# Optimization experiments

Hardware: AMD Instinct MI355X
Metric: run time of the kernel (lower is better)

The kernel has to match this reference:

```python
import jax, jax.numpy as jnp
import numpy as np

N = 512
D = 512
# static upper-triangle pair indices (i < j)
_II, _JJ = np.triu_indices(N, k=1)
_II = jnp.asarray(_II)
_JJ = jnp.asarray(_JJ)


def setup_inputs() -> dict:
    key = jax.random.key(0)
    ks = jax.random.split(key, 9)
    s = 0.02
    return {
        'features': jax.random.normal(ks[0], (N, D), dtype=jnp.float32),
        # relation_classifier: Linear(2D->D), Linear(D->10)
        'cw1': jax.random.normal(ks[1], (2 * D, D), dtype=jnp.float32) * s,
        'cb1': jnp.zeros((D,), dtype=jnp.float32),
        'cw2': jax.random.normal(ks[2], (D, 10), dtype=jnp.float32) * s,
        'cb2': jnp.zeros((10,), dtype=jnp.float32),
        # relation_strength_calc: Linear(2D->D//2), Linear(D//2->1)
        'sw1': jax.random.normal(ks[3], (2 * D, D // 2), dtype=jnp.float32) * s,
        'sb1': jnp.zeros((D // 2,), dtype=jnp.float32),
        'sw2': jax.random.normal(ks[4], (D // 2, 1), dtype=jnp.float32) * s,
        'sb2': jnp.zeros((1,), dtype=jnp.float32),
    }


def reference(features, cw1, cb1, cw2, cb2, sw1, sb1, sw2, sb2):
    # cat([f_i, f_j]) @ W == f_i @ W[:D] + f_j @ W[D:]  (linear-split trick)
    # precompute per-node projections once, then gather per pair
    c_a = features @ cw1[:D]   # [N, D]
    c_b = features @ cw1[D:]   # [N, D]
    s_a = features @ sw1[:D]   # [N, D//2]
    s_b = features @ sw1[D:]   # [N, D//2]

    # classifier path
    h = jax.nn.relu(c_a[_II] + c_b[_JJ] + cb1)          # [P, D]
    relation_types = jax.nn.log_softmax(h @ cw2 + cb2)   # [P, 10]
    most_likely_relations = jnp.argmax(relation_types, axis=-1)  # [P]

    # strength path
    hs = jax.nn.relu(s_a[_II] + s_b[_JJ] + sb1)          # [P, D//2]
    relation_strengths = jax.nn.sigmoid(hs @ sw2 + sb2)   # [P, 1]

    return relation_types, most_likely_relations, relation_strengths
```

## Files before the change

kernel.cpp:

```cpp
#include <hip/hip_runtime.h>
#include <math.h>

#define NN 512
#define DD 512
#define NPAIRS 130816
#define TYPES_OFF 0
#define ARGMAX_OFF 1308160
#define STRENGTH_OFF 1438976


__global__ __launch_bounds__(256) void init_ws_kernel(
    const float* __restrict__ cb1, const float* __restrict__ sb1,
    const float* __restrict__ cw2,
    double* __restrict__ ca_d, double* __restrict__ cb_d,
    float* __restrict__ sa_f, float* __restrict__ sb_f,
    double* __restrict__ cw2d)
{
    int idx = blockIdx.x * 256 + threadIdx.x;
    ca_d[idx] = (double)cb1[idx & 511];
    cb_d[idx] = 0.0;
    if (idx < 131072) {
        sa_f[idx] = sb1[idx & 255];
        sb_f[idx] = 0.f;
    }
    if (idx < 5120) cw2d[idx] = (double)cw2[idx];
}

__global__ __launch_bounds__(256, 4) void proj_kernel(
    const float* __restrict__ F, const float* __restrict__ cw1,
    const float* __restrict__ sw1,
    double* __restrict__ ca_d, double* __restrict__ cb_d,
    float* __restrict__ sa_f, float* __restrict__ sb_f)
{
    __shared__ double sh[2 * 16 * 66];

    const int t = threadIdx.x;
    const int b = blockIdx.x;

    const int am = t & 63, aq = t >> 6;
    const int br = t >> 4, bq = t & 15;
    const int ty = t >> 4, tx = t & 15;

    if (b < 256) {
        const int z  = b >> 7;
        const int r  = b & 127;
        const int m0 = (r >> 4) * 64;
        const int ng = (r & 15) * 64;
        const float* Bp  = (ng < 512) ? cw1 : cw1 + 512 * 512;
        double* outp     = (ng < 512) ? ca_d : cb_d;
        const int coloff = (ng < 512) ? ng : ng - 512;

        double* As = sh;
        double* Bs = sh + 16 * 66;

        double acc[4][4];
        #pragma unroll
        for (int r2 = 0; r2 < 4; ++r2)
            #pragma unroll
            for (int c2 = 0; c2 < 4; ++c2) acc[r2][c2] = 0.0;

        for (int k0 = z * 256; k0 < z * 256 + 256; k0 += 16) {
            float4 fa = *(const float4*)&F [(m0 + am) * 512 + k0 + aq * 4];
            float4 fb = *(const float4*)&Bp[(k0 + br) * 512 + coloff + bq * 4];
            __syncthreads();
            As[(aq * 4 + 0) * 66 + am] = (double)fa.x;
            As[(aq * 4 + 1) * 66 + am] = (double)fa.y;
            As[(aq * 4 + 2) * 66 + am] = (double)fa.z;
            As[(aq * 4 + 3) * 66 + am] = (double)fa.w;
            double2* bd = (double2*)&Bs[br * 66 + bq * 4];
            bd[0] = make_double2((double)fb.x, (double)fb.y);
            bd[1] = make_double2((double)fb.z, (double)fb.w);
            __syncthreads();
            #pragma unroll
            for (int kk = 0; kk < 16; ++kk) {
                double2 a0 = *(double2*)&As[kk * 66 + ty * 4];
                double2 a1 = *(double2*)&As[kk * 66 + ty * 4 + 2];
                double2 b0 = *(double2*)&Bs[kk * 66 + tx * 4];
                double2 b1 = *(double2*)&Bs[kk * 66 + tx * 4 + 2];
                double av[4] = {a0.x, a0.y, a1.x, a1.y};
                double bv[4] = {b0.x, b0.y, b1.x, b1.y};
                #pragma unroll
                for (int r2 = 0; r2 < 4; ++r2)
                    #pragma unroll
                    for (int c2 = 0; c2 < 4; ++c2)
                        acc[r2][c2] = fma(av[r2], bv[c2], acc[r2][c2]);
            }
        }
        #pragma unroll
        for (int r2 = 0; r2 < 4; ++r2)
            #pragma unroll
            for (int c2 = 0; c2 < 4; ++c2)
                unsafeAtomicAdd(&outp[(m0 + ty * 4 + r2) * 512 + coloff + tx * 4 + c2],
                                acc[r2][c2]);
    } else {
        const int b2 = b - 256;
        const int z  = b2 >> 6;
        const int r  = b2 & 63;
        const int m0 = (r >> 3) * 64;
        const int ng = (r & 7) * 64;
        const float* Bp  = (ng < 256) ? sw1 : sw1 + 512 * 256;
        float* outp      = (ng < 256) ? sa_f : sb_f;
        const int coloff = (ng < 256) ? ng : ng - 256;

        float* Asf = (float*)sh;
        float* Bsf = (float*)sh + 16 * 68;

        float acc[4][4];
        #pragma unroll
        for (int r2 = 0; r2 < 4; ++r2)
            #pragma unroll
            for (int c2 = 0; c2 < 4; ++c2) acc[r2][c2] = 0.f;

        for (int k0 = z * 256; k0 < z * 256 + 256; k0 += 16) {
            float4 fa = *(const float4*)&F [(m0 + am) * 512 + k0 + aq * 4];
            float4 fb = *(const float4*)&Bp[(k0 + br) * 256 + coloff + bq * 4];
            __syncthreads();
            Asf[(aq * 4 + 0) * 68 + am] = fa.x;
            Asf[(aq * 4 + 1) * 68 + am] = fa.y;
            Asf[(aq * 4 + 2) * 68 + am] = fa.z;
            Asf[(aq * 4 + 3) * 68 + am] = fa.w;
            *(float4*)&Bsf[br * 68 + bq * 4] = fb;
            __syncthreads();
            #pragma unroll
            for (int kk = 0; kk < 16; ++kk) {
                float4 a4 = *(float4*)&Asf[kk * 68 + ty * 4];
                float4 b4 = *(float4*)&Bsf[kk * 68 + tx * 4];
                float av[4] = {a4.x, a4.y, a4.z, a4.w};
                float bv[4] = {b4.x, b4.y, b4.z, b4.w};
                #pragma unroll
                for (int r2 = 0; r2 < 4; ++r2)
                    #pragma unroll
                    for (int c2 = 0; c2 < 4; ++c2)
                        acc[r2][c2] = fmaf(av[r2], bv[c2], acc[r2][c2]);
            }
        }
        #pragma unroll
        for (int r2 = 0; r2 < 4; ++r2)
            #pragma unroll
            for (int c2 = 0; c2 < 4; ++c2)
                unsafeAtomicAdd(&outp[(m0 + ty * 4 + r2) * 256 + coloff + tx * 4 + c2],
                                acc[r2][c2]);
    }
}

__global__ __launch_bounds__(256, 4) void pair_kernel(
    const double* __restrict__ ca_d, const double* __restrict__ cb_d,
    const float* __restrict__ sa_f, const float* __restrict__ sb_f,
    const double* __restrict__ cw2d, const float* __restrict__ cb2,
    const float* __restrict__ sw2, const float* __restrict__ sb2,
    float* __restrict__ out)
{
    const int b = blockIdx.x;
    int bi = (int)floorf((129.0f - sqrtf(16641.0f - 8.0f * (float)b)) * 0.5f);
    while ((bi + 1) * (129 - (bi + 1)) / 2 <= b) ++bi;
    while (bi * (129 - bi) / 2 > b) --bi;
    const int bj = bi + (b - bi * (129 - bi) / 2);
    const int i0 = bi * 8, j0 = bj * 8;

    const int t = threadIdx.x;
    const int q  = t >> 6;
    const int qu = __builtin_amdgcn_readfirstlane(q);
    const int l = t & 63;
    const int pi = l >> 3, pj = l & 7;
    const int i = i0 + pi, j = j0 + pj;

    __shared__ double smem_d[2176];
    double* sA  = smem_d;
    double* sB  = smem_d + 1088;
    float*  sSa = (float*)smem_d;
    float*  sSb = (float*)smem_d + 2176;
    double* lgbuf = smem_d;
    float*  stbuf = (float*)(smem_d + 1920);

    #pragma unroll
    for (int u = 0; u < 4; ++u) {
        int idx = u * 256 + t;
        int kq  = idx & 15;
        int row = (idx >> 4) & 7;
        int qq  = (idx >> 7) & 3;
        int arr = idx >> 9;
        const float* src = arr ? (sb_f + (j0 + row) * 256) : (sa_f + (i0 + row) * 256);
        float4 v = *(const float4*)(src + qq * 64 + kq * 4);
        float* dst = (arr ? sSb : sSa) + (qq * 8 + row) * 68 + kq * 4;
        *(float4*)dst = v;
    }
    __syncthreads();
    float accs = 0.f;
    {
        const float* sw2q = sw2 + qu * 64;
        const float* ra = sSa + (q * 8 + pi) * 68;
        const float* rb = sSb + (q * 8 + pj) * 68;
        #pragma unroll 16
        for (int kk = 0; kk < 64; ++kk) {
            float h = fmaxf(ra[kk] + rb[kk], 0.f);
            accs = fmaf(h, sw2q[kk], accs);
        }
    }

    double lg[10];
    #pragma unroll
    for (int c = 0; c < 10; ++c) lg[c] = 0.0;
    const double* wq = cw2d + qu * 1280;

    for (int c4 = 0; c4 < 4; ++c4) {
        __syncthreads();
        #pragma unroll
        for (int u = 0; u < 4; ++u) {
            int idx = u * 256 + t;
            int kq  = idx & 15;
            int row = (idx >> 4) & 7;
            int qq  = (idx >> 7) & 3;
            int arr = idx >> 9;
            const double* src = arr ? (cb_d + (j0 + row) * 512) : (ca_d + (i0 + row) * 512);
            double2 v = *(const double2*)(src + qq * 128 + c4 * 32 + kq * 2);
            double* dst = (arr ? sB : sA) + (qq * 8 + row) * 34 + kq * 2;
            *(double2*)dst = v;
        }
        __syncthreads();
        const double* ra = sA + (q * 8 + pi) * 34;
        const double* rb = sB + (q * 8 + pj) * 34;
        const double* wc = wq + c4 * 320;
        #pragma unroll 8
        for (int kk = 0; kk < 32; ++kk) {
            double h = fmax(ra[kk] + rb[kk], 0.0);
            const double* w = wc + kk * 10;
            #pragma unroll
            for (int c = 0; c < 10; ++c) lg[c] = fma(h, w[c], lg[c]);
        }
    }

    __syncthreads();
    if (q > 0) {
        double* dst = lgbuf + ((q - 1) * 64 + l) * 10;
        #pragma unroll
        for (int c = 0; c < 10; ++c) dst[c] = lg[c];
        stbuf[(q - 1) * 64 + l] = accs;
    }
    __syncthreads();
    if (q == 0) {
        #pragma unroll
        for (int w = 0; w < 3; ++w) {
            const double* srcb = lgbuf + (w * 64 + l) * 10;
            #pragma unroll
            for (int c = 0; c < 10; ++c) lg[c] += srcb[c];
        }
        float st = accs + stbuf[l] + stbuf[64 + l] + stbuf[128 + l] + sb2[0];

        #pragma unroll
        for (int c = 0; c < 10; ++c) lg[c] += (double)cb2[c];
        double mx = lg[0]; int am2 = 0;
        #pragma unroll
        for (int c = 1; c < 10; ++c) {
            if (lg[c] > mx) { mx = lg[c]; am2 = c; }
        }
        float tf[10]; float s = 0.f;
        #pragma unroll
        for (int c = 0; c < 10; ++c) { tf[c] = (float)(lg[c] - mx); s += __expf(tf[c]); }
        float ls = __logf(s);

        if (j > i) {
            const int p = i * 511 - (i * (i - 1)) / 2 + (j - i - 1);
            float* tp = out + TYPES_OFF + p * 10;
            #pragma unroll
            for (int c = 0; c < 10; ++c) tp[c] = tf[c] - ls;
            out[ARGMAX_OFF + p] = (float)am2;
            out[STRENGTH_OFF + p] = 1.0f / (1.0f + __expf(-st));
        }
    }
}

extern "C" void kernel_launch(void* const* d_in, const int* in_sizes, int n_in,
                              void* d_out, int out_size, void* d_ws, size_t ws_size,
                              hipStream_t stream) {
    const float* F   = (const float*)d_in[0];
    const float* cw1 = (const float*)d_in[1];
    const float* cb1 = (const float*)d_in[2];
    const float* cw2 = (const float*)d_in[3];
    const float* cb2 = (const float*)d_in[4];
    const float* sw1 = (const float*)d_in[5];
    const float* sb1 = (const float*)d_in[6];
    const float* sw2 = (const float*)d_in[7];
    const float* sb2 = (const float*)d_in[8];
    float* out = (float*)d_out;

    char* ws = (char*)d_ws;
    double* ca_d = (double*)(ws);
    double* cb_d = (double*)(ws + 2097152);
    float*  sa_f = (float*)(ws + 4194304);
    float*  sb_f = (float*)(ws + 4718592);
    double* cw2d = (double*)(ws + 5242880);

    hipLaunchKernelGGL(init_ws_kernel, dim3(1024), dim3(256), 0, stream,
                       cb1, sb1, cw2, ca_d, cb_d, sa_f, sb_f, cw2d);
    hipLaunchKernelGGL(proj_kernel, dim3(384), dim3(256), 0, stream,
                       F, cw1, sw1, ca_d, cb_d, sa_f, sb_f);
    hipLaunchKernelGGL(pair_kernel, dim3(2080), dim3(256), 0, stream,
                       ca_d, cb_d, sa_f, sb_f, cw2d, cb2, sw2, sb2, out);
}
```

Baseline: 164.0 us.

## Drop init kernel and atomics; split-K partials summed in pair kernel

Removes the workspace init kernel and the atomic accumulation in the projection GEMM. Each split-K half now writes its own partial buffer with plain stores, the bias is added in the z=0 half, and the pair kernel sums the two partials when it loads tiles. The projection is rewritten as a per-wave register-tiled GEMM that reads operands straight from global memory with software prefetch instead of going through LDS. This saves one launch and the atomic traffic, but doubles the projection bytes the pair kernel reads and drops LDS reuse in the GEMM.

```diff
diff --git a/kernel.cpp b/kernel.cpp
--- a/kernel.cpp
+++ b/kernel.cpp
@@ -9,143 +9,182 @@
 #define STRENGTH_OFF 1438976
 
 
-__global__ __launch_bounds__(256) void init_ws_kernel(
-    const float* __restrict__ cb1, const float* __restrict__ sb1,
-    const float* __restrict__ cw2,
-    double* __restrict__ ca_d, double* __restrict__ cb_d,
-    float* __restrict__ sa_f, float* __restrict__ sb_f,
-    double* __restrict__ cw2d)
+__device__ __forceinline__ void fma64_step(
+    const float4& a0, const float4& a1,
+    const float4& b0, const float4& b1, const float4& b2, const float4& b3,
+    double acc[2][4])
 {
-    int idx = blockIdx.x * 256 + threadIdx.x;
-    ca_d[idx] = (double)cb1[idx & 511];
-    cb_d[idx] = 0.0;
-    if (idx < 131072) {
-        sa_f[idx] = sb1[idx & 255];
-        sb_f[idx] = 0.f;
-    }
-    if (idx < 5120) cw2d[idx] = (double)cw2[idx];
+    const float av[2][4] = {{a0.x,a0.y,a0.z,a0.w},{a1.x,a1.y,a1.z,a1.w}};
+    const float bv[4][4] = {{b0.x,b0.y,b0.z,b0.w},{b1.x,b1.y,b1.z,b1.w},
+                            {b2.x,b2.y,b2.z,b2.w},{b3.x,b3.y,b3.z,b3.w}};
+    #pragma unroll
+    for (int kk = 0; kk < 4; ++kk) {
+        double ad0 = (double)av[0][kk], ad1 = (double)av[1][kk];
+        #pragma unroll
+        for (int c = 0; c < 4; ++c) {
+            double bd = (double)bv[kk][c];
+            acc[0][c] = fma(ad0, bd, acc[0][c]);
+            acc[1][c] = fma(ad1, bd, acc[1][c]);
+        }
+    }
+}
+
+__device__ __forceinline__ void fma32_step(
+    const float4& a0, const float4& a1,
+    const float4& b0, const float4& b1, const float4& b2, const float4& b3,
+    float acc[2][4])
+{
+    const float av[2][4] = {{a0.x,a0.y,a0.z,a0.w},{a1.x,a1.y,a1.z,a1.w}};
+    const float bv[4][4] = {{b0.x,b0.y,b0.z,b0.w},{b1.x,b1.y,b1.z,b1.w},
+                            {b2.x,b2.y,b2.z,b2.w},{b3.x,b3.y,b3.z,b3.w}};
+    #pragma unroll
+    for (int kk = 0; kk < 4; ++kk) {
+        #pragma unroll
+        for (int c = 0; c < 4; ++c) {
+            acc[0][c] = fmaf(av[0][kk], bv[kk][c], acc[0][c]);
+            acc[1][c] = fmaf(av[1][kk], bv[kk][c], acc[1][c]);
+        }
+    }
 }
 
 __global__ __launch_bounds__(256, 4) void proj_kernel(
     const float* __restrict__ F, const float* __restrict__ cw1,
     const float* __restrict__ sw1,
-    double* __restrict__ ca_d, double* __restrict__ cb_d,
-    float* __restrict__ sa_f, float* __restrict__ sb_f)
+    const float* __restrict__ cb1, const float* __restrict__ sb1,
+    const float* __restrict__ cw2,
+    double* __restrict__ ca0, double* __restrict__ ca1,
+    double* __restrict__ cb0, double* __restrict__ cbp1,
+    float* __restrict__ sa0, float* __restrict__ sa1,
+    float* __restrict__ sb0, float* __restrict__ sbp1,
+    double* __restrict__ cw2d)
 {
-    __shared__ double sh[2 * 16 * 66];
-
     const int t = threadIdx.x;
-    const int b = blockIdx.x;
-
-    const int am = t & 63, aq = t >> 6;
-    const int br = t >> 4, bq = t & 15;
-    const int ty = t >> 4, tx = t & 15;
-
-    if (b < 256) {
-        const int z  = b >> 7;
-        const int r  = b & 127;
-        const int m0 = (r >> 4) * 64;
-        const int ng = (r & 15) * 64;
-        const float* Bp  = (ng < 512) ? cw1 : cw1 + 512 * 512;
-        double* outp     = (ng < 512) ? ca_d : cb_d;
-        const int coloff = (ng < 512) ? ng : ng - 512;
-
-        double* As = sh;
-        double* Bs = sh + 16 * 66;
-
-        double acc[4][4];
-        #pragma unroll
-        for (int r2 = 0; r2 < 4; ++r2)
-            #pragma unroll
-            for (int c2 = 0; c2 < 4; ++c2) acc[r2][c2] = 0.0;
-
-        for (int k0 = z * 256; k0 < z * 256 + 256; k0 += 16) {
-            float4 fa = *(const float4*)&F [(m0 + am) * 512 + k0 + aq * 4];
-            float4 fb = *(const float4*)&Bp[(k0 + br) * 512 + coloff + bq * 4];
-            __syncthreads();
-            As[(aq * 4 + 0) * 66 + am] = (double)fa.x;
-            As[(aq * 4 + 1) * 66 + am] = (double)fa.y;
-            As[(aq * 4 + 2) * 66 + am] = (double)fa.z;
-            As[(aq * 4 + 3) * 66 + am] = (double)fa.w;
-            double2* bd = (double2*)&Bs[br * 66 + bq * 4];
-            bd[0] = make_double2((double)fb.x, (double)fb.y);
-            bd[1] = make_double2((double)fb.z, (double)fb.w);
-            __syncthreads();
-            #pragma unroll
-            for (int kk = 0; kk < 16; ++kk) {
-                double2 a0 = *(double2*)&As[kk * 66 + ty * 4];
-                double2 a1 = *(double2*)&As[kk * 66 + ty * 4 + 2];
-                double2 b0 = *(double2*)&Bs[kk * 66 + tx * 4];
-                double2 b1 = *(double2*)&Bs[kk * 66 + tx * 4 + 2];
-                double av[4] = {a0.x, a0.y, a1.x, a1.y};
-                double bv[4] = {b0.x, b0.y, b1.x, b1.y};
-                #pragma unroll
-                for (int r2 = 0; r2 < 4; ++r2)
-                    #pragma unroll
-                    for (int c2 = 0; c2 < 4; ++c2)
-                        acc[r2][c2] = fma(av[r2], bv[c2], acc[r2][c2]);
+    if (blockIdx.x >= 768) {
+        int idx = (blockIdx.x - 768) * 256 + t;
+        if (idx < 5120) cw2d[idx] = (double)cw2[idx];
+        return;
+    }
+    const int wid  = blockIdx.x * 4 + (t >> 6);
+    const int lane = t & 63;
+    const int mg = lane >> 4;
+    const int nq = lane & 15;
+
+    if (wid < 2048) {
+        const int z  = wid & 1;
+        const int r  = wid >> 1;
+        const int nt = r & 15;
+        const int mt = r >> 4;
+        const int m0 = mt * 8;
+        const int n  = nt * 64;
+        const float* W = (n < 512) ? cw1 : cw1 + 512 * 512;
+        const int n0   = (n < 512) ? n : n - 512;
+        double* outp   = (n < 512) ? (z ? ca1 : ca0) : (z ? cbp1 : cb0);
+        const bool addbias = (z == 0) && (n < 512);
+
+        const int row0 = m0 + mg * 2;
+        const int col0 = n0 + nq * 4;
+        const float* pa0 = F + row0 * 512 + z * 256;
+        const float* pa1 = pa0 + 512;
+        const float* pb  = W + (z * 256) * 512 + col0;
+
+        double acc[2][4];
+        #pragma unroll
+        for (int rr = 0; rr < 2; ++rr)
+            #pragma unroll
+            for (int cc = 0; cc < 4; ++cc) acc[rr][cc] = 0.0;
+
+        float4 a0 = *(const float4*)(pa0);
+        float4 a1 = *(const float4*)(pa1);
+        float4 b0 = *(const float4*)(pb);
+        float4 b1 = *(const float4*)(pb + 512);
+        float4 b2 = *(const float4*)(pb + 1024);
+        float4 b3 = *(const float4*)(pb + 1536);
+        for (int s = 0; s < 63; ++s) {
+            float4 na0 = *(const float4*)(pa0 + (s + 1) * 4);
+            float4 na1 = *(const float4*)(pa1 + (s + 1) * 4);
+            const float* nb = pb + (s + 1) * 2048;
+            float4 nb0 = *(const float4*)(nb);
+            float4 nb1 = *(const float4*)(nb + 512);
+            float4 nb2 = *(const float4*)(nb + 1024);
+            float4 nb3 = *(const float4*)(nb + 1536);
+            fma64_step(a0, a1, b0, b1, b2, b3, acc);
+            a0 = na0; a1 = na1; b0 = nb0; b1 = nb1; b2 = nb2; b3 = nb3;
+        }
+        fma64_step(a0, a1, b0, b1, b2, b3, acc);
+
+        #pragma unroll
+        for (int rr = 0; rr < 2; ++rr) {
+            double v[4];
+            #pragma unroll
+            for (int cc = 0; cc < 4; ++cc) {
+                v[cc] = acc[rr][cc];
+                if (addbias) v[cc] += (double)cb1[col0 + cc];
             }
-        }
-        #pragma unroll
-        for (int r2 = 0; r2 < 4; ++r2)
-            #pragma unroll
-            for (int c2 = 0; c2 < 4; ++c2)
-                unsafeAtomicAdd(&outp[(m0 + ty * 4 + r2) * 512 + coloff + tx * 4 + c2],
-                                acc[r2][c2]);
+            double* dst = outp + (row0 + rr) * 512 + col0;
+            *(double2*)(dst + 0) = make_double2(v[0], v[1]);
+            *(double2*)(dst + 2) = make_double2(v[2], v[3]);
+        }
     } else {
-        const int b2 = b - 256;
-        const int z  = b2 >> 6;
-        const int r  = b2 & 63;
-        const int m0 = (r >> 3) * 64;
-        const int ng = (r & 7) * 64;
-        const float* Bp  = (ng < 256) ? sw1 : sw1 + 512 * 256;
-        float* outp      = (ng < 256) ? sa_f : sb_f;
-        const int coloff = (ng < 256) ? ng : ng - 256;
-
-        float* Asf = (float*)sh;
-        float* Bsf = (float*)sh + 16 * 68;
-
-        float acc[4][4];
-        #pragma unroll
-        for (int r2 = 0; r2 < 4; ++r2)
-            #pragma unroll
-            for (int c2 = 0; c2 < 4; ++c2) acc[r2][c2] = 0.f;
-
-        for (int k0 = z * 256; k0 < z * 256 + 256; k0 += 16) {
-            float4 fa = *(const float4*)&F [(m0 + am) * 512 + k0 + aq * 4];
-            float4 fb = *(const float4*)&Bp[(k0 + br) * 256 + coloff + bq * 4];
-            __syncthreads();
-            Asf[(aq * 4 + 0) * 68 + am] = fa.x;
-            Asf[(aq * 4 + 1) * 68 + am] = fa.y;
-            Asf[(aq * 4 + 2) * 68 + am] = fa.z;
-            Asf[(aq * 4 + 3) * 68 + am] = fa.w;
-            *(float4*)&Bsf[br * 68 + bq * 4] = fb;
-            __syncthreads();
-            #pragma unroll
-            for (int kk = 0; kk < 16; ++kk) {
-                float4 a4 = *(float4*)&Asf[kk * 68 + ty * 4];
-                float4 b4 = *(float4*)&Bsf[kk * 68 + tx * 4];
-                float av[4] = {a4.x, a4.y, a4.z, a4.w};
-                float bv[4] = {b4.x, b4.y, b4.z, b4.w};
-                #pragma unroll
-                for (int r2 = 0; r2 < 4; ++r2)
-                    #pragma unroll
-                    for (int c2 = 0; c2 < 4; ++c2)
-                        acc[r2][c2] = fmaf(av[r2], bv[c2], acc[r2][c2]);
+        const int w2 = wid - 2048;
+        const int z  = w2 & 1;
+        const int r  = w2 >> 1;
+        const int nt = r & 7;
+        const int mt = r >> 3;
+        const int m0 = mt * 8;
+        const int n  = nt * 64;
+        const float* W = (n < 256) ? sw1 : sw1 + 512 * 256;
+        const int n0   = (n < 256) ? n : n - 256;
+        float* outp    = (n < 256) ? (z ? sa1 : sa0) : (z ? sbp1 : sb0);
+        const bool addbias = (z == 0) && (n < 256);
+
+        const int row0 = m0 + mg * 2;
+        const int col0 = n0 + nq * 4;
+        const float* pa0 = F + row0 * 512 + z * 256;
+        const float* pa1 = pa0 + 512;
+        const float* pb  = W + (z * 256) * 256 + col0;
+
+        float acc[2][4];
+        #pragma unroll
+        for (int rr = 0; rr < 2; ++rr)
+            #pragma unroll
+            for (int cc = 0; cc < 4; ++cc) acc[rr][cc] = 0.f;
+
+        float4 a0 = *(const float4*)(pa0);
+        float4 a1 = *(const float4*)(pa1);
+        float4 b0 = *(const float4*)(pb);
+        float4 b1 = *(const float4*)(pb + 256);
+        float4 b2 = *(const float4*)(pb + 512);
+        float4 b3 = *(const float4*)(pb + 768);
+        for (int s = 0; s < 63; ++s) {
+            float4 na0 = *(const float4*)(pa0 + (s + 1) * 4);
+            float4 na1 = *(const float4*)(pa1 + (s + 1) * 4);
+            const float* nb = pb + (s + 1) * 1024;
+            float4 nb0 = *(const float4*)(nb);
+            float4 nb1 = *(const float4*)(nb + 256);
+            float4 nb2 = *(const float4*)(nb + 512);
+            float4 nb3 = *(const float4*)(nb + 768);
+            fma32_step(a0, a1, b0, b1, b2, b3, acc);
+            a0 = na0; a1 = na1; b0 = nb0; b1 = nb1; b2 = nb2; b3 = nb3;
+        }
+        fma32_step(a0, a1, b0, b1, b2, b3, acc);
+
+        #pragma unroll
+        for (int rr = 0; rr < 2; ++rr) {
+            float4 v = make_float4(acc[rr][0], acc[rr][1], acc[rr][2], acc[rr][3]);
+            if (addbias) {
+                v.x += sb1[col0 + 0]; v.y += sb1[col0 + 1];
+                v.z += sb1[col0 + 2]; v.w += sb1[col0 + 3];
             }
-        }
-        #pragma unroll
-        for (int r2 = 0; r2 < 4; ++r2)
-            #pragma unroll
-            for (int c2 = 0; c2 < 4; ++c2)
-                unsafeAtomicAdd(&outp[(m0 + ty * 4 + r2) * 256 + coloff + tx * 4 + c2],
-                                acc[r2][c2]);
+            *(float4*)(outp + (row0 + rr) * 256 + col0) = v;
+        }
     }
 }
 
 __global__ __launch_bounds__(256, 4) void pair_kernel(
-    const double* __restrict__ ca_d, const double* __restrict__ cb_d,
-    const float* __restrict__ sa_f, const float* __restrict__ sb_f,
+    const double* __restrict__ ca0, const double* __restrict__ ca1,
+    const double* __restrict__ cb0, const double* __restrict__ cbp1,
+    const float* __restrict__ sa0, const float* __restrict__ sa1,
+    const float* __restrict__ sb0, const float* __restrict__ sbp1,
     const double* __restrict__ cw2d, const float* __restrict__ cb2,
     const float* __restrict__ sw2, const float* __restrict__ sb2,
     float* __restrict__ out)
@@ -179,8 +218,12 @@
         int row = (idx >> 4) & 7;
         int qq  = (idx >> 7) & 3;
         int arr = idx >> 9;
-        const float* src = arr ? (sb_f + (j0 + row) * 256) : (sa_f + (i0 + row) * 256);
-        float4 v = *(const float4*)(src + qq * 64 + kq * 4);
+        int off = (arr ? (j0 + row) : (i0 + row)) * 256 + qq * 64 + kq * 4;
+        const float* s0 = arr ? sb0 : sa0;
+        const float* s1 = arr ? sbp1 : sa1;
+        float4 v0 = *(const float4*)(s0 + off);
+        float4 v1 = *(const float4*)(s1 + off);
+        float4 v = make_float4(v0.x + v1.x, v0.y + v1.y, v0.z + v1.z, v0.w + v1.w);
         float* dst = (arr ? sSb : sSa) + (qq * 8 + row) * 68 + kq * 4;
         *(float4*)dst = v;
     }
@@ -211,8 +254,12 @@
             int row = (idx >> 4) & 7;
             int qq  = (idx >> 7) & 3;
             int arr = idx >> 9;
-            const double* src = arr ? (cb_d + (j0 + row) * 512) : (ca_d + (i0 + row) * 512);
-            double2 v = *(const double2*)(src + qq * 128 + c4 * 32 + kq * 2);
+            int off = (arr ? (j0 + row) : (i0 + row)) * 512 + qq * 128 + c4 * 32 + kq * 2;
+            const double* d0 = arr ? cb0 : ca0;
+            const double* d1 = arr ? cbp1 : ca1;
+            double2 u0 = *(const double2*)(d0 + off);
+            double2 u1 = *(const double2*)(d1 + off);
+            double2 v = make_double2(u0.x + u1.x, u0.y + u1.y);
             double* dst = (arr ? sB : sA) + (qq * 8 + row) * 34 + kq * 2;
             *(double2*)dst = v;
         }
@@ -284,16 +331,20 @@
     float* out = (float*)d_out;
 
     char* ws = (char*)d_ws;
-    double* ca_d = (double*)(ws);
-    double* cb_d = (double*)(ws + 2097152);
-    float*  sa_f = (float*)(ws + 4194304);
-    float*  sb_f = (float*)(ws + 4718592);
-    double* cw2d = (double*)(ws + 5242880);
-
-    hipLaunchKernelGGL(init_ws_kernel, dim3(1024), dim3(256), 0, stream,
-                       cb1, sb1, cw2, ca_d, cb_d, sa_f, sb_f, cw2d);
-    hipLaunchKernelGGL(proj_kernel, dim3(384), dim3(256), 0, stream,
-                       F, cw1, sw1, ca_d, cb_d, sa_f, sb_f);
+    double* ca0  = (double*)(ws);
+    double* ca1  = (double*)(ws + 2097152);
+    double* cb0  = (double*)(ws + 4194304);
+    double* cbp1 = (double*)(ws + 6291456);
+    float*  sa0  = (float*)(ws + 8388608);
+    float*  sa1  = (float*)(ws + 8912896);
+    float*  sb0  = (float*)(ws + 9437184);
+    float*  sbp1 = (float*)(ws + 9961472);
+    double* cw2d = (double*)(ws + 10485760);
+
+    hipLaunchKernelGGL(proj_kernel, dim3(788), dim3(256), 0, stream,
+                       F, cw1, sw1, cb1, sb1, cw2,
+                       ca0, ca1, cb0, cbp1, sa0, sa1, sb0, sbp1, cw2d);
     hipLaunchKernelGGL(pair_kernel, dim3(2080), dim3(256), 0, stream,
-                       ca_d, cb_d, sa_f, sb_f, cw2d, cb2, sw2, sb2, out);
-}
+                       ca0, ca1, cb0, cbp1, sa0, sa1, sb0, sbp1,
+                       cw2d, cb2, sw2, sb2, out);
+}
```

Result: faster. 153.1 us (-6.6%).

## Fuse workspace init into projection GEMM, drop split-K atomics, prefetch pair tiles

Applied to the files above, without the earlier changes.

Removes the init kernel by folding the bias add and cw2 double conversion into the projection kernel. The projection GEMM switches from a split-K shared-memory tiled scheme with atomic accumulation to per-wave register tiles that read global memory directly, with a two-stage software-pipelined load, and writes results with plain stores. The pair kernel now prefetches the next chunk of double projections into registers while computing the current one. In exchange there is less data reuse through LDS in the GEMM, and the occupancy hint drops to two blocks.

```diff
diff --git a/kernel.cpp b/kernel.cpp
--- a/kernel.cpp
+++ b/kernel.cpp
@@ -9,137 +9,153 @@
 #define STRENGTH_OFF 1438976
 
 
-__global__ __launch_bounds__(256) void init_ws_kernel(
+struct StageC { float4 a0, a1, b0, b1, b2, b3; };
+
+__device__ __forceinline__ void fma64_step(const StageC& s, double acc[2][4]) {
+    const float av[2][4] = {{s.a0.x,s.a0.y,s.a0.z,s.a0.w},{s.a1.x,s.a1.y,s.a1.z,s.a1.w}};
+    const float bv[4][4] = {{s.b0.x,s.b0.y,s.b0.z,s.b0.w},{s.b1.x,s.b1.y,s.b1.z,s.b1.w},
+                            {s.b2.x,s.b2.y,s.b2.z,s.b2.w},{s.b3.x,s.b3.y,s.b3.z,s.b3.w}};
+    #pragma unroll
+    for (int kk = 0; kk < 4; ++kk) {
+        double ad0 = (double)av[0][kk], ad1 = (double)av[1][kk];
+        #pragma unroll
+        for (int c = 0; c < 4; ++c) {
+            double bd = (double)bv[kk][c];
+            acc[0][c] = fma(ad0, bd, acc[0][c]);
+            acc[1][c] = fma(ad1, bd, acc[1][c]);
+        }
+    }
+}
+
+__device__ __forceinline__ void fma32_step(const StageC& s, float acc[2][4]) {
+    const float av[2][4] = {{s.a0.x,s.a0.y,s.a0.z,s.a0.w},{s.a1.x,s.a1.y,s.a1.z,s.a1.w}};
+    const float bv[4][4] = {{s.b0.x,s.b0.y,s.b0.z,s.b0.w},{s.b1.x,s.b1.y,s.b1.z,s.b1.w},
+                            {s.b2.x,s.b2.y,s.b2.z,s.b2.w},{s.b3.x,s.b3.y,s.b3.z,s.b3.w}};
+    #pragma unroll
+    for (int kk = 0; kk < 4; ++kk) {
+        #pragma unroll
+        for (int c = 0; c < 4; ++c) {
+            acc[0][c] = fmaf(av[0][kk], bv[kk][c], acc[0][c]);
+            acc[1][c] = fmaf(av[1][kk], bv[kk][c], acc[1][c]);
+        }
+    }
+}
+
+__global__ __launch_bounds__(256, 2) void proj_kernel(
+    const float* __restrict__ F, const float* __restrict__ cw1,
+    const float* __restrict__ sw1,
     const float* __restrict__ cb1, const float* __restrict__ sb1,
     const float* __restrict__ cw2,
     double* __restrict__ ca_d, double* __restrict__ cb_d,
     float* __restrict__ sa_f, float* __restrict__ sb_f,
     double* __restrict__ cw2d)
 {
-    int idx = blockIdx.x * 256 + threadIdx.x;
-    ca_d[idx] = (double)cb1[idx & 511];
-    cb_d[idx] = 0.0;
-    if (idx < 131072) {
-        sa_f[idx] = sb1[idx & 255];
-        sb_f[idx] = 0.f;
-    }
-    if (idx < 5120) cw2d[idx] = (double)cw2[idx];
-}
-
-__global__ __launch_bounds__(256, 4) void proj_kernel(
-    const float* __restrict__ F, const float* __restrict__ cw1,
-    const float* __restrict__ sw1,
-    double* __restrict__ ca_d, double* __restrict__ cb_d,
-    float* __restrict__ sa_f, float* __restrict__ sb_f)
-{
-    __shared__ double sh[2 * 16 * 66];
-
     const int t = threadIdx.x;
     const int b = blockIdx.x;
-
-    const int am = t & 63, aq = t >> 6;
-    const int br = t >> 4, bq = t & 15;
-    const int ty = t >> 4, tx = t & 15;
+    if (b >= 384) {
+        int idx = (b - 384) * 256 + t;
+        if (idx < 5120) cw2d[idx] = (double)cw2[idx];
+        return;
+    }
+    const int lane = t & 63;
+    const int mg = lane >> 4;
+    const int nq = lane & 15;
 
     if (b < 256) {
-        const int z  = b >> 7;
-        const int r  = b & 127;
-        const int m0 = (r >> 4) * 64;
-        const int ng = (r & 15) * 64;
-        const float* Bp  = (ng < 512) ? cw1 : cw1 + 512 * 512;
-        double* outp     = (ng < 512) ? ca_d : cb_d;
-        const int coloff = (ng < 512) ? ng : ng - 512;
-
-        double* As = sh;
-        double* Bs = sh + 16 * 66;
-
-        double acc[4][4];
-        #pragma unroll
-        for (int r2 = 0; r2 < 4; ++r2)
-            #pragma unroll
-            for (int c2 = 0; c2 < 4; ++c2) acc[r2][c2] = 0.0;
-
-        for (int k0 = z * 256; k0 < z * 256 + 256; k0 += 16) {
-            float4 fa = *(const float4*)&F [(m0 + am) * 512 + k0 + aq * 4];
-            float4 fb = *(const float4*)&Bp[(k0 + br) * 512 + coloff + bq * 4];
-            __syncthreads();
-            As[(aq * 4 + 0) * 66 + am] = (double)fa.x;
-            As[(aq * 4 + 1) * 66 + am] = (double)fa.y;
-            As[(aq * 4 + 2) * 66 + am] = (double)fa.z;
-            As[(aq * 4 + 3) * 66 + am] = (double)fa.w;
-            double2* bd = (double2*)&Bs[br * 66 + bq * 4];
-            bd[0] = make_double2((double)fb.x, (double)fb.y);
-            bd[1] = make_double2((double)fb.z, (double)fb.w);
-            __syncthreads();
-            #pragma unroll
-            for (int kk = 0; kk < 16; ++kk) {
-                double2 a0 = *(double2*)&As[kk * 66 + ty * 4];
-                double2 a1 = *(double2*)&As[kk * 66 + ty * 4 + 2];
-                double2 b0 = *(double2*)&Bs[kk * 66 + tx * 4];
-                double2 b1 = *(double2*)&Bs[kk * 66 + tx * 4 + 2];
-                double av[4] = {a0.x, a0.y, a1.x, a1.y};
-                double bv[4] = {b0.x, b0.y, b1.x, b1.y};
-                #pragma unroll
-                for (int r2 = 0; r2 < 4; ++r2)
-                    #pragma unroll
-                    for (int c2 = 0; c2 < 4; ++c2)
-                        acc[r2][c2] = fma(av[r2], bv[c2], acc[r2][c2]);
+        const int wid = b * 4 + (t >> 6);
+        const int mt = wid >> 4, nt = wid & 15;
+        const int m0 = mt * 8, n = nt * 64;
+        const float* W   = (n < 512) ? cw1 : cw1 + 262144;
+        const int n0     = (n < 512) ? n : n - 512;
+        double* outp     = (n < 512) ? ca_d : cb_d;
+        const bool addb  = (n < 512);
+
+        const int row0 = m0 + mg * 2;
+        const int col0 = n0 + nq * 4;
+        const float* pa0 = F + row0 * 512;
+        const float* pa1 = pa0 + 512;
+        const float* pb  = W + col0;
+
+        double acc[2][4];
+        #pragma unroll
+        for (int r = 0; r < 2; ++r)
+            #pragma unroll
+            for (int c = 0; c < 4; ++c) acc[r][c] = 0.0;
+
+        #define LDC(s) StageC{ *(const float4*)(pa0 + 4*(s)), *(const float4*)(pa1 + 4*(s)), \
+            *(const float4*)(pb + (4*(s)+0)*512), *(const float4*)(pb + (4*(s)+1)*512), \
+            *(const float4*)(pb + (4*(s)+2)*512), *(const float4*)(pb + (4*(s)+3)*512) }
+
+        StageC c0 = LDC(0), c1 = LDC(1);
+        for (int s = 0; s < 126; s += 2) {
+            StageC p0 = LDC(s + 2);
+            StageC p1 = LDC(s + 3);
+            fma64_step(c0, acc);
+            fma64_step(c1, acc);
+            c0 = p0; c1 = p1;
+        }
+        fma64_step(c0, acc);
+        fma64_step(c1, acc);
+        #undef LDC
+
+        #pragma unroll
+        for (int r = 0; r < 2; ++r) {
+            double v[4];
+            #pragma unroll
+            for (int c = 0; c < 4; ++c) {
+                v[c] = acc[r][c];
+                if (addb) v[c] += (double)cb1[col0 + c];
             }
-        }
-        #pragma unroll
-        for (int r2 = 0; r2 < 4; ++r2)
-            #pragma unroll
-            for (int c2 = 0; c2 < 4; ++c2)
-                unsafeAtomicAdd(&outp[(m0 + ty * 4 + r2) * 512 + coloff + tx * 4 + c2],
-                                acc[r2][c2]);
+            double* dst = outp + (row0 + r) * 512 + col0;
+            *(double2*)(dst + 0) = make_double2(v[0], v[1]);
+            *(double2*)(dst + 2) = make_double2(v[2], v[3]);
+        }
     } else {
-        const int b2 = b - 256;
-        const int z  = b2 >> 6;
-        const int r  = b2 & 63;
-        const int m0 = (r >> 3) * 64;
-        const int ng = (r & 7) * 64;
-        const float* Bp  = (ng < 256) ? sw1 : sw1 + 512 * 256;
-        float* outp      = (ng < 256) ? sa_f : sb_f;
-        const int coloff = (ng < 256) ? ng : ng - 256;
-
-        float* Asf = (float*)sh;
-        float* Bsf = (float*)sh + 16 * 68;
-
-        float acc[4][4];
-        #pragma unroll
-        for (int r2 = 0; r2 < 4; ++r2)
-            #pragma unroll
-            for (int c2 = 0; c2 < 4; ++c2) acc[r2][c2] = 0.f;
-
-        for (int k0 = z * 256; k0 < z * 256 + 256; k0 += 16) {
-            float4 fa = *(const float4*)&F [(m0 + am) * 512 + k0 + aq * 4];
-            float4 fb = *(const float4*)&Bp[(k0 + br) * 256 + coloff + bq * 4];
-            __syncthreads();
-            Asf[(aq * 4 + 0) * 68 + am] = fa.x;
-            Asf[(aq * 4 + 1) * 68 + am] = fa.y;
-            Asf[(aq * 4 + 2) * 68 + am] = fa.z;
-            Asf[(aq * 4 + 3) * 68 + am] = fa.w;
-            *(float4*)&Bsf[br * 68 + bq * 4] = fb;
-            __syncthreads();
-            #pragma unroll
-            for (int kk = 0; kk < 16; ++kk) {
-                float4 a4 = *(float4*)&Asf[kk * 68 + ty * 4];
-                float4 b4 = *(float4*)&Bsf[kk * 68 + tx * 4];
-                float av[4] = {a4.x, a4.y, a4.z, a4.w};
-                float bv[4] = {b4.x, b4.y, b4.z, b4.w};
-                #pragma unroll
-                for (int r2 = 0; r2 < 4; ++r2)
-                    #pragma unroll
-                    for (int c2 = 0; c2 < 4; ++c2)
-                        acc[r2][c2] = fmaf(av[r2], bv[c2], acc[r2][c2]);
+        const int wid = (b - 256) * 4 + (t >> 6);
+        const int mt = wid >> 3, nt = wid & 7;
+        const int m0 = mt * 8, n = nt * 64;
+        const float* W  = (n < 256) ? sw1 : sw1 + 131072;
+        const int n0    = (n < 256) ? n : n - 256;
+        float* outp     = (n < 256) ? sa_f : sb_f;
+        const bool addb = (n < 256);
+
+        const int row0 = m0 + mg * 2;
+        const int col0 = n0 + nq * 4;
+        const float* pa0 = F + row0 * 512;
+        const float* pa1 = pa0 + 512;
+        const float* pb  = W + col0;
+
+        float acc[2][4];
+        #pragma unroll
+        for (int r = 0; r < 2; ++r)
+            #pragma unroll
+            for (int c = 0; c < 4; ++c) acc[r][c] = 0.f;
+
+        #define LDS4(s) StageC{ *(const float4*)(pa0 + 4*(s)), *(const float4*)(pa1 + 4*(s)), \
+            *(const float4*)(pb + (4*(s)+0)*256), *(const float4*)(pb + (4*(s)+1)*256), \
+            *(const float4*)(pb + (4*(s)+2)*256), *(const float4*)(pb + (4*(s)+3)*256) }
+
+        StageC c0 = LDS4(0), c1 = LDS4(1);
+        for (int s = 0; s < 126; s += 2) {
+            StageC p0 = LDS4(s + 2);
+            StageC p1 = LDS4(s + 3);
+            fma32_step(c0, acc);
+            fma32_step(c1, acc);
+            c0 = p0; c1 = p1;
+        }
+        fma32_step(c0, acc);
+        fma32_step(c1, acc);
+        #undef LDS4
+
+        #pragma unroll
+        for (int r = 0; r < 2; ++r) {
+            float4 v = make_float4(acc[r][0], acc[r][1], acc[r][2], acc[r][3]);
+            if (addb) {
+                v.x += sb1[col0 + 0]; v.y += sb1[col0 + 1];
+                v.z += sb1[col0 + 2]; v.w += sb1[col0 + 3];
             }
-        }
-        #pragma unroll
-        for (int r2 = 0; r2 < 4; ++r2)
-            #pragma unroll
-            for (int c2 = 0; c2 < 4; ++c2)
-                unsafeAtomicAdd(&outp[(m0 + ty * 4 + r2) * 256 + coloff + tx * 4 + c2],
-                                acc[r2][c2]);
+            *(float4*)(outp + (row0 + r) * 256 + col0) = v;
+        }
     }
 }
 
@@ -172,19 +188,33 @@
     double* lgbuf = smem_d;
     float*  stbuf = (float*)(smem_d + 1920);
 
+    const int kq  = t & 15;
+    const int row = (t >> 4) & 7;
+    const int qq0 = (t >> 7) & 3;
+
     #pragma unroll
     for (int u = 0; u < 4; ++u) {
-        int idx = u * 256 + t;
-        int kq  = idx & 15;
-        int row = (idx >> 4) & 7;
-        int qq  = (idx >> 7) & 3;
-        int arr = idx >> 9;
+        int qqu = (qq0 + 2 * u) & 3;
+        int arr = u >> 1;
         const float* src = arr ? (sb_f + (j0 + row) * 256) : (sa_f + (i0 + row) * 256);
-        float4 v = *(const float4*)(src + qq * 64 + kq * 4);
-        float* dst = (arr ? sSb : sSa) + (qq * 8 + row) * 68 + kq * 4;
+        float4 v = *(const float4*)(src + qqu * 64 + kq * 4);
+        float* dst = (arr ? sSb : sSa) + (qqu * 8 + row) * 68 + kq * 4;
         *(float4*)dst = v;
     }
     __syncthreads();
+
+    const double* pfbase[4];
+    #pragma unroll
+    for (int u = 0; u < 4; ++u) {
+        int qqu = (qq0 + 2 * u) & 3;
+        int arr = u >> 1;
+        pfbase[u] = (arr ? (cb_d + (j0 + row) * 512) : (ca_d + (i0 + row) * 512))
+                    + qqu * 128 + kq * 2;
+    }
+    double2 pf[4];
+    #pragma unroll
+    for (int u = 0; u < 4; ++u) pf[u] = *(const double2*)(pfbase[u]);
+
     float accs = 0.f;
     {
         const float* sw2q = sw2 + qu * 64;
@@ -206,17 +236,17 @@
         __syncthreads();
         #pragma unroll
         for (int u = 0; u < 4; ++u) {
-            int idx = u * 256 + t;
-            int kq  = idx & 15;
-            int row = (idx >> 4) & 7;
-            int qq  = (idx >> 7) & 3;
-            int arr = idx >> 9;
-            const double* src = arr ? (cb_d + (j0 + row) * 512) : (ca_d + (i0 + row) * 512);
-            double2 v = *(const double2*)(src + qq * 128 + c4 * 32 + kq * 2);
-            double* dst = (arr ? sB : sA) + (qq * 8 + row) * 34 + kq * 2;
-            *(double2*)dst = v;
+            int qqu = (qq0 + 2 * u) & 3;
+            int arr = u >> 1;
+            double* dst = (arr ? sB : sA) + (qqu * 8 + row) * 34 + kq * 2;
+            *(double2*)dst = pf[u];
         }
         __syncthreads();
+        if (c4 < 3) {
+            #pragma unroll
+            for (int u = 0; u < 4; ++u)
+                pf[u] = *(const double2*)(pfbase[u] + (c4 + 1) * 32);
+        }
         const double* ra = sA + (q * 8 + pi) * 34;
         const double* rb = sB + (q * 8 + pj) * 34;
         const double* wc = wq + c4 * 320;
@@ -290,10 +320,9 @@
     float*  sb_f = (float*)(ws + 4718592);
     double* cw2d = (double*)(ws + 5242880);
 
-    hipLaunchKernelGGL(init_ws_kernel, dim3(1024), dim3(256), 0, stream,
-                       cb1, sb1, cw2, ca_d, cb_d, sa_f, sb_f, cw2d);
-    hipLaunchKernelGGL(proj_kernel, dim3(384), dim3(256), 0, stream,
-                       F, cw1, sw1, ca_d, cb_d, sa_f, sb_f);
+    hipLaunchKernelGGL(proj_kernel, dim3(404), dim3(256), 0, stream,
+                       F, cw1, sw1, cb1, sb1, cw2,
+                       ca_d, cb_d, sa_f, sb_f, cw2d);
     hipLaunchKernelGGL(pair_kernel, dim3(2080), dim3(256), 0, stream,
                        ca_d, cb_d, sa_f, sb_f, cw2d, cb2, sw2, sb2, out);
 }
```

New measurement: 175.0 us. +6.7%, slower.
